# Optimization experiments

Hardware: AMD Instinct MI355X
Metric: run time of the kernel (lower is better)

## Reference

```python
import jax, jax.numpy as jnp
import numpy as np

N_NODES = 50000


def _sage_conv(x, src, dst, Wl, Wr, b):
    """SAGEConv with mean aggregation: lin_l(mean_j x_j) + lin_r(x_i) + b."""
    msgs = x[src]                                                # [E, Din] gather
    agg = jax.ops.segment_sum(msgs, dst, num_segments=N_NODES)  # [N, Din] scatter-add
    cnt = jax.ops.segment_sum(jnp.ones((src.shape[0], 1), x.dtype), dst,
                              num_segments=N_NODES)             # [N, 1]
    agg = agg / jnp.maximum(cnt, 1.0)                           # mean
    return agg @ Wl.T + x @ Wr.T + b                            # [N, Dout]


def setup_inputs() -> dict:
    key = jax.random.key(0)
    ks = jax.random.split(key, 8)
    d_in, d_h = 64, 128
    x = jax.random.normal(ks[0], (N_NODES, d_in), dtype=jnp.float32)
    edge_index = jax.random.randint(ks[1], (2, 800000), 0, N_NODES, dtype=jnp.int32)
    s1 = 1.0 / np.sqrt(d_in)
    s2 = 1.0 / np.sqrt(d_h)
    return {
        "x": x,
        "edge_index": edge_index,
        "Wl1": jax.random.normal(ks[2], (d_h, d_in), dtype=jnp.float32) * s1,
        "Wr1": jax.random.normal(ks[3], (d_h, d_in), dtype=jnp.float32) * s1,
        "b1": jnp.zeros((d_h,), dtype=jnp.float32),
        "Wl2": jax.random.normal(ks[4], (d_h, d_h), dtype=jnp.float32) * s2,
        "Wr2": jax.random.normal(ks[5], (d_h, d_h), dtype=jnp.float32) * s2,
        "b2": jnp.zeros((d_h,), dtype=jnp.float32),
    }


def reference(x, edge_index, Wl1, Wr1, b1, Wl2, Wr2, b2):
    src, dst = edge_index[0], edge_index[1]
    # layer 1: conv -> dropout(eval: identity) -> ReLU
    h = jax.nn.relu(_sage_conv(x, src, dst, Wl1, Wr1, b1))
    # layer 2
    h = jax.nn.relu(_sage_conv(h, src, dst, Wl2, Wr2, b2))
    return h
```

## Files before the change

### kernel.cpp

```cpp
#include <hip/hip_runtime.h>

#define N_NODES 50000
#define NBUCK 391
#define BCAP 4096
#define BSHIFT 12

typedef __attribute__((ext_vector_type(8))) short short8;
typedef __attribute__((ext_vector_type(4))) float floatx4;

static __device__ __forceinline__ unsigned short f2bf(float f) {
  unsigned int u = __builtin_bit_cast(unsigned int, f);
  u += 0x7fff + ((u >> 16) & 1);
  return (unsigned short)(u >> 16);
}
static __device__ __forceinline__ float bf2f(unsigned short s) {
  unsigned int u = ((unsigned int)s) << 16;
  return __builtin_bit_cast(float, u);
}


__global__ void __launch_bounds__(256) prep(
    const float* __restrict__ x,
    const float* __restrict__ Wl1, const float* __restrict__ Wr1,
    const float* __restrict__ Wl2, const float* __restrict__ Wr2,
    unsigned short* __restrict__ A1, unsigned short* __restrict__ W1,
    unsigned short* __restrict__ W2, int* __restrict__ bucket_cur, int n) {
  const int gid = blockIdx.x * 256 + threadIdx.x;
  const int gsz = gridDim.x * 256;
  for (int i = gid; i < n * 64; i += gsz)
    A1[(size_t)(i >> 6) * 128 + 64 + (i & 63)] = f2bf(x[i]);
  for (int i = gid; i < 128 * 128; i += gsz) {
    int c = i >> 7, k = i & 127;
    W1[i] = f2bf(k < 64 ? Wl1[c * 64 + k] : Wr1[c * 64 + k - 64]);
  }
  for (int i = gid; i < 128 * 256; i += gsz) {
    int c = i >> 8, k = i & 255;
    W2[i] = f2bf(k < 128 ? Wl2[c * 128 + k] : Wr2[c * 128 + k - 128]);
  }
  for (int i = gid; i < NBUCK; i += gsz) bucket_cur[i] = 0;
}


__global__ void __launch_bounds__(1024) bucket_scatter(
    const int* __restrict__ src, const int* __restrict__ dst,
    int* __restrict__ bucket_cur, int* __restrict__ buf, int E) {
  __shared__ int hist[NBUCK];
  __shared__ int base_s[NBUCK];
  int t = threadIdx.x;
  for (int i = t; i < NBUCK; i += 1024) hist[i] = 0;
  __syncthreads();
  int e0 = blockIdx.x * 4096;
  int sv[4], dv[4], bv[4];
#pragma unroll
  for (int p = 0; p < 4; ++p) {
    int e = e0 + p * 1024 + t;
    if (e < E) {
      sv[p] = src[e];
      dv[p] = dst[e];
      bv[p] = dv[p] >> 7;
      atomicAdd(&hist[bv[p]], 1);
    } else bv[p] = -1;
  }
  __syncthreads();
  for (int i = t; i < NBUCK; i += 1024) {
    int c = hist[i];
    base_s[i] = c > 0 ? atomicAdd(&bucket_cur[i], c) : 0;
  }
  __syncthreads();
  for (int i = t; i < NBUCK; i += 1024) hist[i] = 0;
  __syncthreads();
#pragma unroll
  for (int p = 0; p < 4; ++p) {
    if (bv[p] >= 0) {
      int sub = base_s[bv[p]] + atomicAdd(&hist[bv[p]], 1);
      if (sub < BCAP) buf[(bv[p] << BSHIFT) + sub] = (sv[p] << 7) | (dv[p] & 127);
    }
  }
}


__global__ void __launch_bounds__(1024) bucket_csr_agg64(
    int* __restrict__ buf, const int* __restrict__ bucket_cur,
    int* __restrict__ row_start, int* __restrict__ row_cnt,
    unsigned short* __restrict__ A1, int n) {
  __shared__ int eb[BCAP];
  __shared__ int cnt[128];
  __shared__ int tmp[128];
  __shared__ int cur[128];
  const int t = threadIdx.x;
  const int b = blockIdx.x;
  const int node0 = b << 7;
  const int len = min(bucket_cur[b], BCAP);
  int* reg = buf + (b << BSHIFT);
  if (t < 128) cnt[t] = 0;
  __syncthreads();
  for (int i = t; i < len; i += 1024) {
    int p = reg[i];
    eb[i] = p;
    atomicAdd(&cnt[p & 127], 1);
  }
  __syncthreads();
  if (t < 128) tmp[t] = cnt[t];
  __syncthreads();
#pragma unroll
  for (int off = 1; off < 128; off <<= 1) {
    int u = (t >= off && t < 128) ? tmp[t - off] : 0;
    __syncthreads();
    if (t < 128) tmp[t] += u;
    __syncthreads();
  }
  if (t < 128) {
    int ex = tmp[t] - cnt[t];
    cur[t] = ex;
    int nd = node0 + t;
    if (nd < n) {
      row_start[nd] = (b << BSHIFT) + ex;
      row_cnt[nd] = cnt[t];
    }
  }
  __syncthreads();
  for (int i = t; i < len; i += 1024) {
    int p = eb[i];
    int sub = atomicAdd(&cur[p & 127], 1);
    reg[sub] = p >> 7;
  }
  __syncthreads();
  const int lane = t & 63;
  const int wv = t >> 6;
  for (int loc = wv; loc < 128; loc += 16) {
    int nd = node0 + loc;
    if (nd >= n) break;
    int cn = cnt[loc];
    const int* sp = reg + (tmp[loc] - cn);
    float a0 = 0.f, a1 = 0.f, a2 = 0.f, a3 = 0.f;
    int e = 0;
    for (; e + 4 <= cn; e += 4) {
      int s0 = sp[e];
      int s1 = sp[e + 1];
      int s2 = sp[e + 2];
      int s3 = sp[e + 3];
      a0 += bf2f(A1[(size_t)s0 * 128 + 64 + lane]);
      a1 += bf2f(A1[(size_t)s1 * 128 + 64 + lane]);
      a2 += bf2f(A1[(size_t)s2 * 128 + 64 + lane]);
      a3 += bf2f(A1[(size_t)s3 * 128 + 64 + lane]);
    }
    for (; e < cn; ++e) a0 += bf2f(A1[(size_t)sp[e] * 128 + 64 + lane]);
    A1[(size_t)nd * 128 + lane] = f2bf((a0 + a1 + a2 + a3) * (1.0f / (float)max(cn, 1)));
  }
}


__global__ void agg_mean128(unsigned short* __restrict__ A2,
    const int* __restrict__ row_start, const int* __restrict__ row_cnt,
    const int* __restrict__ srcs, int n) {
  int wid = (blockIdx.x * blockDim.x + threadIdx.x) >> 6;
  int lane = threadIdx.x & 63;
  if (wid >= n) return;
  int start = row_start[wid];
  int cnt = row_cnt[wid];
  float ax = 0.f, ay = 0.f, bx = 0.f, by = 0.f;
  float cx = 0.f, cy = 0.f, dx = 0.f, dy = 0.f;
  int e = 0;
  for (; e + 4 <= cnt; e += 4) {
    int s0 = srcs[start + e];
    int s1 = srcs[start + e + 1];
    int s2 = srcs[start + e + 2];
    int s3 = srcs[start + e + 3];
    unsigned int u0 = *(const unsigned int*)(A2 + (size_t)s0 * 256 + 128 + lane * 2);
    unsigned int u1 = *(const unsigned int*)(A2 + (size_t)s1 * 256 + 128 + lane * 2);
    unsigned int u2 = *(const unsigned int*)(A2 + (size_t)s2 * 256 + 128 + lane * 2);
    unsigned int u3 = *(const unsigned int*)(A2 + (size_t)s3 * 256 + 128 + lane * 2);
    ax += bf2f((unsigned short)u0); ay += bf2f((unsigned short)(u0 >> 16));
    bx += bf2f((unsigned short)u1); by += bf2f((unsigned short)(u1 >> 16));
    cx += bf2f((unsigned short)u2); cy += bf2f((unsigned short)(u2 >> 16));
    dx += bf2f((unsigned short)u3); dy += bf2f((unsigned short)(u3 >> 16));
  }
  for (; e < cnt; ++e) {
    unsigned int u0 = *(const unsigned int*)(A2 + (size_t)srcs[start + e] * 256 + 128 + lane * 2);
    ax += bf2f((unsigned short)u0); ay += bf2f((unsigned short)(u0 >> 16));
  }
  float inv = 1.0f / (float)max(cnt, 1);
  unsigned int packed = (unsigned int)f2bf((ax + bx + cx + dx) * inv)
                      | ((unsigned int)f2bf((ay + by + cy + dy) * inv) << 16);
  *(unsigned int*)(A2 + (size_t)wid * 256 + lane * 2) = packed;
}


template<int KP, bool BF_OUT>
__global__ void __launch_bounds__(256) mfma_gemm(
    const unsigned short* __restrict__ A, const unsigned short* __restrict__ W,
    const float* __restrict__ bias, unsigned short* __restrict__ outb,
    float* __restrict__ outf, int n, int ostride, int ocol) {
  const int lane = threadIdx.x & 63;
  const int wv = threadIdx.x >> 6;
  const int m = lane & 15;
  const int q = lane >> 4;
  const int r0 = blockIdx.x * 128 + wv * 32;

  floatx4 acc[2][8];
#pragma unroll
  for (int rt = 0; rt < 2; ++rt)
#pragma unroll
    for (int ct = 0; ct < 8; ++ct) acc[rt][ct] = (floatx4){0.f, 0.f, 0.f, 0.f};

  int ra = r0 + m;      if (ra > n - 1) ra = n - 1;
  int rb = r0 + 16 + m; if (rb > n - 1) rb = n - 1;
  const unsigned short* Arow0 = A + (size_t)ra * KP + q * 8;
  const unsigned short* Arow1 = A + (size_t)rb * KP + q * 8;
  const unsigned short* Wrow  = W + (size_t)m * KP + q * 8;

#pragma unroll 1
  for (int kc = 0; kc < KP / 32; ++kc) {
    short8 a0 = *(const short8*)(Arow0 + kc * 32);
    short8 a1 = *(const short8*)(Arow1 + kc * 32);
#pragma unroll
    for (int ct = 0; ct < 8; ++ct) {
      short8 wf = *(const short8*)(Wrow + (size_t)ct * 16 * KP + kc * 32);
      acc[0][ct] = __builtin_amdgcn_mfma_f32_16x16x32_bf16(a0, wf, acc[0][ct], 0, 0, 0);
      acc[1][ct] = __builtin_amdgcn_mfma_f32_16x16x32_bf16(a1, wf, acc[1][ct], 0, 0, 0);
    }
  }

  float bv[8];
#pragma unroll
  for (int ct = 0; ct < 8; ++ct) bv[ct] = bias[ct * 16 + m];

#pragma unroll
  for (int rt = 0; rt < 2; ++rt) {
#pragma unroll
    for (int j = 0; j < 4; ++j) {
      int row = r0 + rt * 16 + q * 4 + j;
      if (row < n) {
#pragma unroll
        for (int ct = 0; ct < 8; ++ct) {
          float v = acc[rt][ct][j] + bv[ct];
          v = v > 0.f ? v : 0.f;
          int col = ct * 16 + m;
          if (BF_OUT) outb[(size_t)row * ostride + ocol + col] = f2bf(v);
          else        outf[(size_t)row * ostride + col] = v;
        }
      }
    }
  }
}


extern "C" void kernel_launch(void* const* d_in, const int* in_sizes, int n_in,
                              void* d_out, int out_size, void* d_ws, size_t ws_size,
                              hipStream_t stream) {
  const int N = N_NODES;
  const int E = in_sizes[1] / 2;
  const float* x   = (const float*)d_in[0];
  const int*   src = (const int*)d_in[1];
  const int*   dst = src + E;
  const float* Wl1 = (const float*)d_in[2];
  const float* Wr1 = (const float*)d_in[3];
  const float* b1  = (const float*)d_in[4];
  const float* Wl2 = (const float*)d_in[5];
  const float* Wr2 = (const float*)d_in[6];
  const float* b2  = (const float*)d_in[7];
  float* out = (float*)d_out;

  unsigned short* A1 = (unsigned short*)d_ws;
  unsigned short* A2 = A1 + (size_t)N * 128;
  unsigned short* W1 = A2 + (size_t)N * 256;
  unsigned short* W2 = W1 + 128 * 128;
  int* row_start  = (int*)(W2 + 128 * 256);
  int* row_cnt    = row_start + N;
  int* bucket_cur = row_cnt + N;
  int* buf        = bucket_cur + 392;

  prep<<<512, 256, 0, stream>>>(x, Wl1, Wr1, Wl2, Wr2, A1, W1, W2, bucket_cur, N);
  bucket_scatter<<<(E + 4095) / 4096, 1024, 0, stream>>>(src, dst, bucket_cur, buf, E);
  bucket_csr_agg64<<<NBUCK, 1024, 0, stream>>>(buf, bucket_cur, row_start, row_cnt, A1, N);

  int gb = (N + 127) / 128;
  mfma_gemm<128, true><<<gb, 256, 0, stream>>>(A1, W1, b1, A2, nullptr, N, 256, 128);

  int ab = (N * 64 + 255) / 256;
  agg_mean128<<<ab, 256, 0, stream>>>(A2, row_start, row_cnt, buf, N);
  mfma_gemm<256, false><<<gb, 256, 0, stream>>>(A2, W2, b2, nullptr, out, N, 128, 0);
}
```

Measured before the change: 208.1 us.

## Fuse prep into bucket scatter and vectorize neighbor gathers with short8 loads

The prep kernel (bf16 conversion of x and weights) is merged into the bucket-scatter kernel, and the bucket counter reset moves to a hipMemsetAsync, removing one launch. Both mean-aggregation loops now have each lane load 8 bf16 values at once (16-byte loads), with several edges handled in parallel across lane groups and combined by xor-shuffle reductions. This cuts the number of memory instructions per gathered row and adds edge-level parallelism, at the cost of shuffle overhead and idle lanes when degree is not a multiple of the group count.

```diff
diff --git a/kernel.cpp b/kernel.cpp
--- a/kernel.cpp
+++ b/kernel.cpp
@@ -19,14 +19,17 @@
 }
 
 
-__global__ void __launch_bounds__(256) prep(
+__global__ void __launch_bounds__(1024) prep_scatter(
     const float* __restrict__ x,
     const float* __restrict__ Wl1, const float* __restrict__ Wr1,
     const float* __restrict__ Wl2, const float* __restrict__ Wr2,
     unsigned short* __restrict__ A1, unsigned short* __restrict__ W1,
-    unsigned short* __restrict__ W2, int* __restrict__ bucket_cur, int n) {
-  const int gid = blockIdx.x * 256 + threadIdx.x;
-  const int gsz = gridDim.x * 256;
+    unsigned short* __restrict__ W2,
+    const int* __restrict__ src, const int* __restrict__ dst,
+    int* __restrict__ bucket_cur, int* __restrict__ buf, int E, int n) {
+  const int t = threadIdx.x;
+  const int gid = blockIdx.x * 1024 + t;
+  const int gsz = gridDim.x * 1024;
   for (int i = gid; i < n * 64; i += gsz)
     A1[(size_t)(i >> 6) * 128 + 64 + (i & 63)] = f2bf(x[i]);
   for (int i = gid; i < 128 * 128; i += gsz) {
@@ -37,16 +40,9 @@
     int c = i >> 8, k = i & 255;
     W2[i] = f2bf(k < 128 ? Wl2[c * 128 + k] : Wr2[c * 128 + k - 128]);
   }
-  for (int i = gid; i < NBUCK; i += gsz) bucket_cur[i] = 0;
-}
-
-
-__global__ void __launch_bounds__(1024) bucket_scatter(
-    const int* __restrict__ src, const int* __restrict__ dst,
-    int* __restrict__ bucket_cur, int* __restrict__ buf, int E) {
+
   __shared__ int hist[NBUCK];
   __shared__ int base_s[NBUCK];
-  int t = threadIdx.x;
   for (int i = t; i < NBUCK; i += 1024) hist[i] = 0;
   __syncthreads();
   int e0 = blockIdx.x * 4096;
@@ -127,25 +123,37 @@
   __syncthreads();
   const int lane = t & 63;
   const int wv = t >> 6;
+  const int eq = lane >> 3;
+  const int cl = lane & 7;
   for (int loc = wv; loc < 128; loc += 16) {
     int nd = node0 + loc;
     if (nd >= n) break;
     int cn = cnt[loc];
     const int* sp = reg + (tmp[loc] - cn);
-    float a0 = 0.f, a1 = 0.f, a2 = 0.f, a3 = 0.f;
-    int e = 0;
-    for (; e + 4 <= cn; e += 4) {
-      int s0 = sp[e];
-      int s1 = sp[e + 1];
-      int s2 = sp[e + 2];
-      int s3 = sp[e + 3];
-      a0 += bf2f(A1[(size_t)s0 * 128 + 64 + lane]);
-      a1 += bf2f(A1[(size_t)s1 * 128 + 64 + lane]);
-      a2 += bf2f(A1[(size_t)s2 * 128 + 64 + lane]);
-      a3 += bf2f(A1[(size_t)s3 * 128 + 64 + lane]);
-    }
-    for (; e < cn; ++e) a0 += bf2f(A1[(size_t)sp[e] * 128 + 64 + lane]);
-    A1[(size_t)nd * 128 + lane] = f2bf((a0 + a1 + a2 + a3) * (1.0f / (float)max(cn, 1)));
+    float acc[8];
+#pragma unroll
+    for (int j = 0; j < 8; ++j) acc[j] = 0.f;
+    for (int e = 0; e < cn; e += 8) {
+      if (e + eq < cn) {
+        int s = sp[e + eq];
+        short8 v = *(const short8*)(A1 + (size_t)s * 128 + 64 + cl * 8);
+#pragma unroll
+        for (int j = 0; j < 8; ++j) acc[j] += bf2f((unsigned short)v[j]);
+      }
+    }
+#pragma unroll
+    for (int j = 0; j < 8; ++j) {
+      acc[j] += __shfl_xor(acc[j], 8, 64);
+      acc[j] += __shfl_xor(acc[j], 16, 64);
+      acc[j] += __shfl_xor(acc[j], 32, 64);
+    }
+    if (eq == 0) {
+      float inv = 1.0f / (float)max(cn, 1);
+      short8 o;
+#pragma unroll
+      for (int j = 0; j < 8; ++j) o[j] = (short)f2bf(acc[j] * inv);
+      *(short8*)(A1 + (size_t)nd * 128 + cl * 8) = o;
+    }
   }
 }
 
@@ -158,31 +166,31 @@
   if (wid >= n) return;
   int start = row_start[wid];
   int cnt = row_cnt[wid];
-  float ax = 0.f, ay = 0.f, bx = 0.f, by = 0.f;
-  float cx = 0.f, cy = 0.f, dx = 0.f, dy = 0.f;
-  int e = 0;
-  for (; e + 4 <= cnt; e += 4) {
-    int s0 = srcs[start + e];
-    int s1 = srcs[start + e + 1];
-    int s2 = srcs[start + e + 2];
-    int s3 = srcs[start + e + 3];
-    unsigned int u0 = *(const unsigned int*)(A2 + (size_t)s0 * 256 + 128 + lane * 2);
-    unsigned int u1 = *(const unsigned int*)(A2 + (size_t)s1 * 256 + 128 + lane * 2);
-    unsigned int u2 = *(const unsigned int*)(A2 + (size_t)s2 * 256 + 128 + lane * 2);
-    unsigned int u3 = *(const unsigned int*)(A2 + (size_t)s3 * 256 + 128 + lane * 2);
-    ax += bf2f((unsigned short)u0); ay += bf2f((unsigned short)(u0 >> 16));
-    bx += bf2f((unsigned short)u1); by += bf2f((unsigned short)(u1 >> 16));
-    cx += bf2f((unsigned short)u2); cy += bf2f((unsigned short)(u2 >> 16));
-    dx += bf2f((unsigned short)u3); dy += bf2f((unsigned short)(u3 >> 16));
-  }
-  for (; e < cnt; ++e) {
-    unsigned int u0 = *(const unsigned int*)(A2 + (size_t)srcs[start + e] * 256 + 128 + lane * 2);
-    ax += bf2f((unsigned short)u0); ay += bf2f((unsigned short)(u0 >> 16));
-  }
-  float inv = 1.0f / (float)max(cnt, 1);
-  unsigned int packed = (unsigned int)f2bf((ax + bx + cx + dx) * inv)
-                      | ((unsigned int)f2bf((ay + by + cy + dy) * inv) << 16);
-  *(unsigned int*)(A2 + (size_t)wid * 256 + lane * 2) = packed;
+  const int eq = lane >> 4;
+  const int cl = lane & 15;
+  float acc[8];
+#pragma unroll
+  for (int j = 0; j < 8; ++j) acc[j] = 0.f;
+  for (int e = 0; e < cnt; e += 4) {
+    if (e + eq < cnt) {
+      int s = srcs[start + e + eq];
+      short8 v = *(const short8*)(A2 + (size_t)s * 256 + 128 + cl * 8);
+#pragma unroll
+      for (int j = 0; j < 8; ++j) acc[j] += bf2f((unsigned short)v[j]);
+    }
+  }
+#pragma unroll
+  for (int j = 0; j < 8; ++j) {
+    acc[j] += __shfl_xor(acc[j], 16, 64);
+    acc[j] += __shfl_xor(acc[j], 32, 64);
+  }
+  if (eq == 0) {
+    float inv = 1.0f / (float)max(cnt, 1);
+    short8 o;
+#pragma unroll
+    for (int j = 0; j < 8; ++j) o[j] = (short)f2bf(acc[j] * inv);
+    *(short8*)(A2 + (size_t)wid * 256 + cl * 8) = o;
+  }
 }
 
 
@@ -270,8 +278,10 @@
   int* bucket_cur = row_cnt + N;
   int* buf        = bucket_cur + 392;
 
-  prep<<<512, 256, 0, stream>>>(x, Wl1, Wr1, Wl2, Wr2, A1, W1, W2, bucket_cur, N);
-  bucket_scatter<<<(E + 4095) / 4096, 1024, 0, stream>>>(src, dst, bucket_cur, buf, E);
+  hipMemsetAsync(bucket_cur, 0, NBUCK * sizeof(int), stream);
+  int sb = (E + 4095) / 4096;
+  prep_scatter<<<sb, 1024, 0, stream>>>(x, Wl1, Wr1, Wl2, Wr2, A1, W1, W2,
+                                        src, dst, bucket_cur, buf, E, N);
   bucket_csr_agg64<<<NBUCK, 1024, 0, stream>>>(buf, bucket_cur, row_start, row_cnt, A1, N);
 
   int gb = (N + 127) / 128;
```

New measurement: 200.6 us. 1.04x faster.
